# Kernel tuning notes

Hardware: AMD Instinct MI355X
Metric: run time of the kernel (lower is better)

## Reference

```python
import jax, jax.numpy as jnp
import numpy as np

# Lloyd-Max (Max 1960) optimal 16-level quantizer for N(0,1), bits=4
_CODEBOOK_4 = np.array([-2.7326, -2.069, -1.6181, -1.2562, -0.9424, -0.6568,
                        -0.3881, -0.1284, 0.1284, 0.3881, 0.6568, 0.9424,
                        1.2562, 1.6181, 2.069, 2.7326], dtype=np.float32)
DIM = 256


def setup_inputs() -> dict:
    key = jax.random.key(0)
    kx, kq = jax.random.split(key)
    x = jax.random.normal(kx, (4, 4096, DIM), dtype=jnp.float32)
    # orthogonal rotation via QR of a Gaussian matrix (mirrors torch.linalg.qr)
    rotation, _ = jnp.linalg.qr(jax.random.normal(kq, (DIM, DIM), dtype=jnp.float32))
    codebook = jnp.asarray(_CODEBOOK_4)
    return {"x": x, "rotation": rotation, "codebook": codebook}


def reference(x, rotation, codebook):
    shape = x.shape
    d = shape[-1]
    sqrt_d = jnp.sqrt(jnp.asarray(d, dtype=x.dtype))
    x_flat = x.reshape(-1, d)                                   # (N, d)
    x_norm = jnp.maximum(
        jnp.linalg.norm(x_flat, axis=-1, keepdims=True), 1e-8)  # (N, 1)
    u = x_flat / x_norm                                         # unit vectors
    y_scaled = (u @ rotation.T) * sqrt_d                        # ~N(0,1) coords
    # nearest codebook entry per scalar coordinate: (N, d, K) -> argmin over K
    idx = jnp.argmin(jnp.abs(y_scaled[..., None] - codebook), axis=-1)
    y_hat = codebook[idx] / sqrt_d                              # (N, d)
    x_hat = (y_hat @ rotation) * x_norm                         # de-rotate, rescale
    return x_hat.reshape(shape)
```

## Files before the change

### kernel.cpp

```cpp
#include <hip/hip_runtime.h>

typedef _Float16 f16;
typedef _Float16 f16x4 __attribute__((ext_vector_type(4)));
typedef _Float16 f16x8 __attribute__((ext_vector_type(8)));
typedef float f32x16 __attribute__((ext_vector_type(16)));
typedef float f32x4 __attribute__((ext_vector_type(4)));

#define APITCH 264

__global__ void prep_kernel(const float* __restrict__ R, f16* __restrict__ ws) {
  f16* W1h = ws;
  f16* W1l = ws + 65536;
  f16* W2h = ws + 131072;
  const int f = blockIdx.x;
  const int g = f >> 4, ks16 = f & 15;
  const int t = threadIdx.x;
  const int l = t >> 3, j = t & 7;
  const int col = 32 * g + (l & 31);
  const int k = 16 * ks16 + 8 * (l >> 5) + j;
  float v1 = R[col * 256 + k] * 256.0f;
  f16 h = (f16)v1;
  f16 lo = (f16)(v1 - (float)h);
  W1h[f * 512 + t] = h;
  W1l[f * 512 + t] = lo;
  W2h[f * 512 + t] = (f16)R[k * 256 + col];
}

__global__ __launch_bounds__(512, 4) void tq_main(
    const float* __restrict__ X, const float* __restrict__ CB,
    const f16* __restrict__ ws, float* __restrict__ OUT) {
  __shared__ f16 A1h[32][APITCH];
  __shared__ f16 A1l[32][APITCH];
  __shared__ float pn[16][32];
  __shared__ float s1s[32], s2s[32];

  const int tid = threadIdx.x;
  const int lane = tid & 63;
  const int wv = tid >> 6;
  const int lrow = lane & 31;
  const int kg = lane >> 5;
  const long row0 = (long)blockIdx.x * 32;

  const f16* W1h = ws;
  const f16* W1l = ws + 65536;
  const f16* W2h = ws + 131072;

  const int r = tid >> 4, q = tid & 15;
  const float* xp = X + (row0 + r) * 256 + q * 16;
  float xa[16];
  #pragma unroll
  for (int i = 0; i < 4; ++i) {
    f32x4 v = ((const f32x4*)xp)[i];
    xa[4 * i] = v.x; xa[4 * i + 1] = v.y; xa[4 * i + 2] = v.z; xa[4 * i + 3] = v.w;
  }
  float ss = 0.f;
  #pragma unroll
  for (int i = 0; i < 16; ++i) ss += xa[i] * xa[i];
  pn[q][r] = ss;
  __syncthreads();
  if (tid < 32) {
    float s = 0.f;
    #pragma unroll
    for (int i = 0; i < 16; ++i) s += pn[i][tid];
    float nrm = fmaxf(sqrtf(s), 1e-8f);
    s1s[tid] = 4096.0f / nrm;
    s2s[tid] = nrm * 0.0625f;
  }
  __syncthreads();

  {
    float s1f = s1s[r];
    #pragma unroll
    for (int c8 = 0; c8 < 2; ++c8) {
      f16x8 h, l;
      #pragma unroll
      for (int j = 0; j < 8; ++j) {
        float a = xa[c8 * 8 + j] * s1f;
        f16 hh = (f16)a;
        h[j] = hh;
        l[j] = (f16)(a - (float)hh);
      }
      *(f16x8*)&A1h[r][q * 16 + c8 * 8] = h;
      *(f16x8*)&A1l[r][q * 16 + c8 * 8] = l;
    }
  }
  __syncthreads();

  const int fb = wv * 16;
  const int lofs = lane * 8;
  f16x8 bh = *(const f16x8*)(W1h + fb * 512 + lofs);
  f16x8 bl = *(const f16x8*)(W1l + fb * 512 + lofs);
  f32x16 zv;
  #pragma unroll
  for (int i = 0; i < 16; ++i) zv[i] = 0.0f;
  f32x16 accH = zv, accL = zv;
  #pragma unroll 4
  for (int ks = 0; ks < 16; ++ks) {
    f16x8 cbh = bh, cbl = bl;
    if (ks < 15) {
      bh = *(const f16x8*)(W1h + (fb + ks + 1) * 512 + lofs);
      bl = *(const f16x8*)(W1l + (fb + ks + 1) * 512 + lofs);
    }
    const int k0 = ks * 16 + kg * 8;
    f16x8 ah = *(const f16x8*)&A1h[lrow][k0];
    f16x8 al = *(const f16x8*)&A1l[lrow][k0];
    accH = __builtin_amdgcn_mfma_f32_32x32x16_f16(ah, cbh, accH, 0, 0, 0);
    accL = __builtin_amdgcn_mfma_f32_32x32x16_f16(al, cbh, accL, 0, 0, 0);
    accH = __builtin_amdgcn_mfma_f32_32x32x16_f16(ah, cbl, accH, 0, 0, 0);
    accL = __builtin_amdgcn_mfma_f32_32x32x16_f16(al, cbl, accL, 0, 0, 0);
  }
  f32x16 acc;
  #pragma unroll
  for (int i = 0; i < 16; ++i) acc[i] = accH[i] + accL[i];

  __syncthreads();

  float cbf[16];
  #pragma unroll
  for (int i = 0; i < 16; ++i) cbf[i] = CB[i];
  float M[15];
  #pragma unroll
  for (int t = 0; t < 15; ++t) M[t] = 65536.0f * (0.5f * (cbf[t] + cbf[t + 1]));
  unsigned int cpk[8];
  #pragma unroll
  for (int i = 0; i < 8; ++i) {
    unsigned short lb = __builtin_bit_cast(unsigned short, (f16)cbf[2 * i]);
    unsigned short hb = __builtin_bit_cast(unsigned short, (f16)cbf[2 * i + 1]);
    cpk[i] = ((unsigned int)hb << 16) | (unsigned int)lb;
  }

  f16 (*Qs)[APITCH] = A1h;
  #pragma unroll
  for (int rr = 0; rr < 16; ++rr) {
    float y = acc[rr];
    int row = 4 * kg + (rr & 3) + 8 * (rr >> 2);
    int kk = 32 * wv + lrow;
    bool b3 = y > M[7];
    float m2 = b3 ? M[11] : M[3];
    bool b2 = y > m2;
    float m1 = b3 ? (b2 ? M[13] : M[9]) : (b2 ? M[5] : M[1]);
    bool b1 = y > m1;
    float m0 = b1 ? (b3 ? (b2 ? M[14] : M[10]) : (b2 ? M[6] : M[2]))
                  : (b3 ? (b2 ? M[12] : M[8]) : (b2 ? M[4] : M[0]));
    bool b0 = y > m0;
    unsigned int pp = b3 ? (b2 ? (b1 ? cpk[7] : cpk[6]) : (b1 ? cpk[5] : cpk[4]))
                         : (b2 ? (b1 ? cpk[3] : cpk[2]) : (b1 ? cpk[1] : cpk[0]));
    unsigned short qb = (unsigned short)(b0 ? (pp >> 16) : (pp & 0xFFFFu));
    Qs[row][kk] = __builtin_bit_cast(f16, qb);
  }
  __syncthreads();

  f16x8 b2 = *(const f16x8*)(W2h + fb * 512 + lofs);
  f32x16 acc2 = zv;
  #pragma unroll 4
  for (int ks = 0; ks < 16; ++ks) {
    f16x8 cb2 = b2;
    if (ks < 15) b2 = *(const f16x8*)(W2h + (fb + ks + 1) * 512 + lofs);
    f16x8 qa = *(const f16x8*)&Qs[lrow][ks * 16 + kg * 8];
    acc2 = __builtin_amdgcn_mfma_f32_32x32x16_f16(qa, cb2, acc2, 0, 0, 0);
  }

  #pragma unroll
  for (int rr = 0; rr < 16; ++rr) {
    int row = 4 * kg + (rr & 3) + 8 * (rr >> 2);
    int col = 32 * wv + lrow;
    OUT[(row0 + row) * 256 + col] = acc2[rr] * s2s[row];
  }
}

#define FB_APITCH 264
#define FB_B1PITCH 40
#define FB_B2PITCH 264

__global__ __launch_bounds__(256, 1) void tq_main_fb(
    const float* __restrict__ X, const float* __restrict__ R,
    const float* __restrict__ CB, float* __restrict__ OUT) {
  __shared__ f16 A1h[64][FB_APITCH];
  __shared__ f16 A1l[64][FB_APITCH];
  __shared__ f16 Qs[64][FB_APITCH];
  __shared__ f32x4 Braw[2624];
  __shared__ float pn[4][64];
  __shared__ float s1s[64];
  __shared__ float s2s[64];

  f16 (*B1h)[FB_B1PITCH] = (f16(*)[FB_B1PITCH])Braw;
  f16 (*B1l)[FB_B1PITCH] = (f16(*)[FB_B1PITCH])((char*)Braw + 20480);
  f16 (*B2h)[FB_B2PITCH] = (f16(*)[FB_B2PITCH])Braw;

  const int tid = threadIdx.x;
  const int lane = tid & 63;
  const int wv = tid >> 6;
  const int lrow = lane & 31;
  const int kg = lane >> 5;
  const long row0 = (long)blockIdx.x * 64;

  float cbf[16];
  #pragma unroll
  for (int i = 0; i < 16; ++i) cbf[i] = CB[i];
  float M[15];
  #pragma unroll
  for (int t = 0; t < 15; ++t) M[t] = 65536.0f * (0.5f * (cbf[t] + cbf[t + 1]));
  unsigned int cpk[8];
  #pragma unroll
  for (int i = 0; i < 8; ++i) {
    unsigned short lb = __builtin_bit_cast(unsigned short, (f16)cbf[2 * i]);
    unsigned short hb = __builtin_bit_cast(unsigned short, (f16)cbf[2 * i + 1]);
    cpk[i] = ((unsigned int)hb << 16) | (unsigned int)lb;
  }

  const int xrow = tid >> 2, xq = tid & 3;
  const float* xp = X + (row0 + xrow) * 256 + xq * 64;
  float xa[64];
  #pragma unroll
  for (int i = 0; i < 16; ++i) {
    f32x4 v = ((const f32x4*)xp)[i];
    xa[4 * i] = v.x; xa[4 * i + 1] = v.y; xa[4 * i + 2] = v.z; xa[4 * i + 3] = v.w;
  }
  float ss = 0.f;
  #pragma unroll
  for (int i = 0; i < 64; ++i) ss += xa[i] * xa[i];
  pn[xq][xrow] = ss;
  __syncthreads();
  if (tid < 64) {
    float s = pn[0][tid] + pn[1][tid] + pn[2][tid] + pn[3][tid];
    float nrm = fmaxf(sqrtf(s), 1e-8f);
    s1s[tid] = 4096.0f / nrm;
    s2s[tid] = nrm * 0.0625f;
  }
  __syncthreads();

  {
    float s1f = s1s[xrow];
    #pragma unroll
    for (int c8 = 0; c8 < 8; ++c8) {
      f16x8 h, l;
      #pragma unroll
      for (int j = 0; j < 8; ++j) {
        float a = xa[c8 * 8 + j] * s1f;
        f16 hh = (f16)a;
        h[j] = hh;
        l[j] = (f16)(a - (float)hh);
      }
      *(f16x8*)&A1h[xrow][xq * 64 + c8 * 8] = h;
      *(f16x8*)&A1l[xrow][xq * 64 + c8 * 8] = l;
    }
  }

  f32x4 pf[8];
  #pragma unroll
  for (int q = 0; q < 8; ++q) {
    int c = q * 256 + tid;
    pf[q] = *(const f32x4*)&R[(long)(c >> 3) * 256 + ((c & 7) * 4)];
  }

  f32x16 zv;
  #pragma unroll
  for (int i = 0; i < 16; ++i) zv[i] = 0.0f;
  f32x16 acc[2][2];
  acc[0][0] = zv; acc[0][1] = zv; acc[1][0] = zv; acc[1][1] = zv;

  for (int kp = 0; kp < 8; ++kp) {
    __syncthreads();
    #pragma unroll
    for (int q = 0; q < 8; ++q) {
      int c = q * 256 + tid;
      int n = c >> 3, k4 = (c & 7) * 4;
      f16x4 h, l;
      #pragma unroll
      for (int j = 0; j < 4; ++j) {
        float sv = pf[q][j] * 256.0f;
        f16 hh = (f16)sv;
        h[j] = hh;
        l[j] = (f16)(sv - (float)hh);
      }
      *(f16x4*)&B1h[n][k4] = h;
      *(f16x4*)&B1l[n][k4] = l;
    }
    __syncthreads();
    if (kp < 7) {
      #pragma unroll
      for (int q = 0; q < 8; ++q) {
        int c = q * 256 + tid;
        pf[q] = *(const f32x4*)&R[(long)(c >> 3) * 256 + (kp + 1) * 32 + ((c & 7) * 4)];
      }
    }
    #pragma unroll
    for (int ks = 0; ks < 2; ++ks) {
      const int k0 = kp * 32 + ks * 16 + kg * 8;
      const int lk = ks * 16 + kg * 8;
      f16x8 ah[2], al[2], bhf[2], blf[2];
      #pragma unroll
      for (int m = 0; m < 2; ++m) {
        ah[m] = *(const f16x8*)&A1h[32 * m + lrow][k0];
        al[m] = *(const f16x8*)&A1l[32 * m + lrow][k0];
      }
      #pragma unroll
      for (int n = 0; n < 2; ++n) {
        int col = 64 * wv + 32 * n + lrow;
        bhf[n] = *(const f16x8*)&B1h[col][lk];
        blf[n] = *(const f16x8*)&B1l[col][lk];
      }
      #pragma unroll
      for (int m = 0; m < 2; ++m)
        #pragma unroll
        for (int n = 0; n < 2; ++n) {
          acc[m][n] = __builtin_amdgcn_mfma_f32_32x32x16_f16(ah[m], bhf[n], acc[m][n], 0, 0, 0);
          acc[m][n] = __builtin_amdgcn_mfma_f32_32x32x16_f16(al[m], bhf[n], acc[m][n], 0, 0, 0);
          acc[m][n] = __builtin_amdgcn_mfma_f32_32x32x16_f16(ah[m], blf[n], acc[m][n], 0, 0, 0);
          acc[m][n] = __builtin_amdgcn_mfma_f32_32x32x16_f16(al[m], blf[n], acc[m][n], 0, 0, 0);
        }
    }
  }

  #pragma unroll
  for (int q = 0; q < 8; ++q) {
    int c = q * 256 + tid;
    pf[q] = *(const f32x4*)&R[(long)(c >> 6) * 256 + ((c & 63) * 4)];
  }

  #pragma unroll
  for (int m = 0; m < 2; ++m)
    #pragma unroll
    for (int n = 0; n < 2; ++n)
      #pragma unroll
      for (int rr = 0; rr < 16; ++rr) {
        float y = acc[m][n][rr];
        int row = 32 * m + 4 * kg + (rr & 3) + 8 * (rr >> 2);
        int kk = 64 * wv + 32 * n + lrow;
        bool b3 = y > M[7];
        float m2 = b3 ? M[11] : M[3];
        bool b2 = y > m2;
        float m1 = b3 ? (b2 ? M[13] : M[9]) : (b2 ? M[5] : M[1]);
        bool b1 = y > m1;
        float m0 = b1 ? (b3 ? (b2 ? M[14] : M[10]) : (b2 ? M[6] : M[2]))
                      : (b3 ? (b2 ? M[12] : M[8]) : (b2 ? M[4] : M[0]));
        bool b0 = y > m0;
        unsigned int pp = b3 ? (b2 ? (b1 ? cpk[7] : cpk[6]) : (b1 ? cpk[5] : cpk[4]))
                             : (b2 ? (b1 ? cpk[3] : cpk[2]) : (b1 ? cpk[1] : cpk[0]));
        unsigned short qb = (unsigned short)(b0 ? (pp >> 16) : (pp & 0xFFFFu));
        Qs[row][kk] = __builtin_bit_cast(f16, qb);
      }
  __syncthreads();

  f32x16 acc2[2][2];
  acc2[0][0] = zv; acc2[0][1] = zv; acc2[1][0] = zv; acc2[1][1] = zv;

  for (int kp = 0; kp < 8; ++kp) {
    if (kp) __syncthreads();
    #pragma unroll
    for (int q = 0; q < 8; ++q) {
      int c = q * 256 + tid;
      int k = c >> 6, n4 = (c & 63) * 4;
      f16x4 h;
      #pragma unroll
      for (int j = 0; j < 4; ++j) h[j] = (f16)pf[q][j];
      *(f16x4*)&B2h[k][n4] = h;
    }
    __syncthreads();
    if (kp < 7) {
      #pragma unroll
      for (int q = 0; q < 8; ++q) {
        int c = q * 256 + tid;
        pf[q] = *(const f32x4*)&R[(long)((kp + 1) * 32 + (c >> 6)) * 256 + ((c & 63) * 4)];
      }
    }
    #pragma unroll
    for (int ks = 0; ks < 2; ++ks) {
      const int k0 = kp * 32 + ks * 16 + kg * 8;
      const int lk = ks * 16 + kg * 8;
      f16x8 qa[2], bb[2];
      #pragma unroll
      for (int m = 0; m < 2; ++m) qa[m] = *(const f16x8*)&Qs[32 * m + lrow][k0];
      #pragma unroll
      for (int n = 0; n < 2; ++n) {
        int colg = 64 * wv + 32 * n + lrow;
        #pragma unroll
        for (int j = 0; j < 8; ++j) bb[n][j] = B2h[lk + j][colg];
      }
      #pragma unroll
      for (int m = 0; m < 2; ++m)
        #pragma unroll
        for (int n = 0; n < 2; ++n)
          acc2[m][n] = __builtin_amdgcn_mfma_f32_32x32x16_f16(qa[m], bb[n], acc2[m][n], 0, 0, 0);
    }
  }

  #pragma unroll
  for (int m = 0; m < 2; ++m)
    #pragma unroll
    for (int n = 0; n < 2; ++n)
      #pragma unroll
      for (int rr = 0; rr < 16; ++rr) {
        int row = 32 * m + 4 * kg + (rr & 3) + 8 * (rr >> 2);
        int col = 64 * wv + 32 * n + lrow;
        OUT[(row0 + row) * 256 + col] = acc2[m][n][rr] * s2s[row];
      }
}

extern "C" void kernel_launch(void* const* d_in, const int* in_sizes, int n_in,
                              void* d_out, int out_size, void* d_ws, size_t ws_size,
                              hipStream_t stream) {
  const float* X = (const float*)d_in[0];
  const float* R = (const float*)d_in[1];
  const float* CB = (const float*)d_in[2];
  float* OUT = (float*)d_out;
  const int nrows = in_sizes[0] / 256;

  if (ws_size >= 3u * 65536u * sizeof(f16)) {
    f16* ws = (f16*)d_ws;
    prep_kernel<<<128, 512, 0, stream>>>(R, ws);
    tq_main<<<nrows / 32, 512, 0, stream>>>(X, CB, ws, OUT);
  } else {
    tq_main_fb<<<nrows / 64, 256, 0, stream>>>(X, R, CB, OUT);
  }
}
```

Before: 28.13 us.

## Restage prep via LDS, shuffle row norms, deepen weight prefetch with dual accumulators

The prep kernel now stages 32 rotation rows in shared memory and writes the fragmented f16 weights with vector stores. It runs 8 blocks of 1024 threads, and the workspace regions are padded so the prefetch can run past the end. The main kernel computes row norms with wave shuffles instead of a shared-memory reduction, which removes two barriers. It also fully unrolls both MFMA loops with two- and four-deep weight prefetch, issues the second GEMM's weight loads before the quantize phase, and splits the second GEMM across two accumulators to break the dependency chain. The cost is more registers and extra reads into the padding past each weight region.

```diff
diff --git a/kernel.cpp b/kernel.cpp
--- a/kernel.cpp
+++ b/kernel.cpp
@@ -7,23 +7,53 @@
 typedef float f32x4 __attribute__((ext_vector_type(4)));
 
 #define APITCH 264
-
-__global__ void prep_kernel(const float* __restrict__ R, f16* __restrict__ ws) {
+#define WREG 67584
+
+__global__ __launch_bounds__(1024) void prep_kernel(const float* __restrict__ R,
+                                                    f16* __restrict__ ws) {
+  __shared__ float Lrs[32][260];
+  const int g = blockIdx.x;
+  const int t = threadIdx.x;
   f16* W1h = ws;
-  f16* W1l = ws + 65536;
-  f16* W2h = ws + 131072;
-  const int f = blockIdx.x;
-  const int g = f >> 4, ks16 = f & 15;
-  const int t = threadIdx.x;
-  const int l = t >> 3, j = t & 7;
-  const int col = 32 * g + (l & 31);
-  const int k = 16 * ks16 + 8 * (l >> 5) + j;
-  float v1 = R[col * 256 + k] * 256.0f;
-  f16 h = (f16)v1;
-  f16 lo = (f16)(v1 - (float)h);
-  W1h[f * 512 + t] = h;
-  W1l[f * 512 + t] = lo;
-  W2h[f * 512 + t] = (f16)R[k * 256 + col];
+  f16* W1l = ws + WREG;
+  f16* W2h = ws + 2 * WREG;
+
+  #pragma unroll
+  for (int it = 0; it < 2; ++it) {
+    int c = it * 1024 + t;
+    int row = c >> 6, c4 = (c & 63) * 4;
+    f32x4 v = *(const f32x4*)&R[(long)(32 * g + row) * 256 + c4];
+    *(f32x4*)&Lrs[row][c4] = v;
+  }
+  __syncthreads();
+
+  {
+    int f_loc = t >> 6, l = t & 63;
+    int k0 = 16 * f_loc + 8 * (l >> 5);
+    const float* src = &Lrs[l & 31][k0];
+    f16x8 h, lo;
+    #pragma unroll
+    for (int j = 0; j < 8; ++j) {
+      float v = src[j] * 256.0f;
+      f16 hh = (f16)v;
+      h[j] = hh;
+      lo[j] = (f16)(v - (float)hh);
+    }
+    long o = (long)(g * 16 + f_loc) * 512 + l * 8;
+    *(f16x8*)(W1h + o) = h;
+    *(f16x8*)(W1l + o) = lo;
+  }
+
+  {
+    int gp = t >> 7, e = (t >> 6) & 1, l = t & 63;
+    int lr0 = 16 * e + 8 * (l >> 5);
+    int col = 32 * gp + (l & 31);
+    f16x8 h;
+    #pragma unroll
+    for (int j = 0; j < 8; ++j) h[j] = (f16)Lrs[lr0 + j][col];
+    long o = (long)(gp * 16 + 2 * g + e) * 512 + l * 8;
+    *(f16x8*)(W2h + o) = h;
+  }
 }
 
 __global__ __launch_bounds__(512, 4) void tq_main(
@@ -31,8 +61,7 @@
     const f16* __restrict__ ws, float* __restrict__ OUT) {
   __shared__ f16 A1h[32][APITCH];
   __shared__ f16 A1l[32][APITCH];
-  __shared__ float pn[16][32];
-  __shared__ float s1s[32], s2s[32];
+  __shared__ float s2s[32];
 
   const int tid = threadIdx.x;
   const int lane = tid & 63;
@@ -42,8 +71,8 @@
   const long row0 = (long)blockIdx.x * 32;
 
   const f16* W1h = ws;
-  const f16* W1l = ws + 65536;
-  const f16* W2h = ws + 131072;
+  const f16* W1l = ws + WREG;
+  const f16* W2h = ws + 2 * WREG;
 
   const int r = tid >> 4, q = tid & 15;
   const float* xp = X + (row0 + r) * 256 + q * 16;
@@ -56,62 +85,75 @@
   float ss = 0.f;
   #pragma unroll
   for (int i = 0; i < 16; ++i) ss += xa[i] * xa[i];
-  pn[q][r] = ss;
-  __syncthreads();
-  if (tid < 32) {
-    float s = 0.f;
-    #pragma unroll
-    for (int i = 0; i < 16; ++i) s += pn[i][tid];
-    float nrm = fmaxf(sqrtf(s), 1e-8f);
-    s1s[tid] = 4096.0f / nrm;
-    s2s[tid] = nrm * 0.0625f;
-  }
-  __syncthreads();
-
-  {
-    float s1f = s1s[r];
-    #pragma unroll
-    for (int c8 = 0; c8 < 2; ++c8) {
-      f16x8 h, l;
-      #pragma unroll
-      for (int j = 0; j < 8; ++j) {
-        float a = xa[c8 * 8 + j] * s1f;
-        f16 hh = (f16)a;
-        h[j] = hh;
-        l[j] = (f16)(a - (float)hh);
-      }
-      *(f16x8*)&A1h[r][q * 16 + c8 * 8] = h;
-      *(f16x8*)&A1l[r][q * 16 + c8 * 8] = l;
-    }
-  }
-  __syncthreads();
-
-  const int fb = wv * 16;
-  const int lofs = lane * 8;
-  f16x8 bh = *(const f16x8*)(W1h + fb * 512 + lofs);
-  f16x8 bl = *(const f16x8*)(W1l + fb * 512 + lofs);
+  ss += __shfl_xor(ss, 8, 16);
+  ss += __shfl_xor(ss, 4, 16);
+  ss += __shfl_xor(ss, 2, 16);
+  ss += __shfl_xor(ss, 1, 16);
+  float nrm = fmaxf(sqrtf(ss), 1e-8f);
+  float s1f = 4096.0f / nrm;
+  if (q == 0) s2s[r] = nrm * 0.0625f;
+
+  #pragma unroll
+  for (int c8 = 0; c8 < 2; ++c8) {
+    f16x8 h, l;
+    #pragma unroll
+    for (int j = 0; j < 8; ++j) {
+      float a = xa[c8 * 8 + j] * s1f;
+      f16 hh = (f16)a;
+      h[j] = hh;
+      l[j] = (f16)(a - (float)hh);
+    }
+    *(f16x8*)&A1h[r][q * 16 + c8 * 8] = h;
+    *(f16x8*)&A1l[r][q * 16 + c8 * 8] = l;
+  }
+  __syncthreads();
+
+  const f16* W1hp = W1h + (long)(wv * 16) * 512 + lane * 8;
+  const f16* W1lp = W1l + (long)(wv * 16) * 512 + lane * 8;
+  f16x8 bh0 = *(const f16x8*)(W1hp);
+  f16x8 bl0 = *(const f16x8*)(W1lp);
+  f16x8 bh1 = *(const f16x8*)(W1hp + 512);
+  f16x8 bl1 = *(const f16x8*)(W1lp + 512);
+
   f32x16 zv;
   #pragma unroll
   for (int i = 0; i < 16; ++i) zv[i] = 0.0f;
   f32x16 accH = zv, accL = zv;
-  #pragma unroll 4
-  for (int ks = 0; ks < 16; ++ks) {
-    f16x8 cbh = bh, cbl = bl;
-    if (ks < 15) {
-      bh = *(const f16x8*)(W1h + (fb + ks + 1) * 512 + lofs);
-      bl = *(const f16x8*)(W1l + (fb + ks + 1) * 512 + lofs);
-    }
-    const int k0 = ks * 16 + kg * 8;
-    f16x8 ah = *(const f16x8*)&A1h[lrow][k0];
-    f16x8 al = *(const f16x8*)&A1l[lrow][k0];
-    accH = __builtin_amdgcn_mfma_f32_32x32x16_f16(ah, cbh, accH, 0, 0, 0);
-    accL = __builtin_amdgcn_mfma_f32_32x32x16_f16(al, cbh, accL, 0, 0, 0);
-    accH = __builtin_amdgcn_mfma_f32_32x32x16_f16(ah, cbl, accH, 0, 0, 0);
-    accL = __builtin_amdgcn_mfma_f32_32x32x16_f16(al, cbl, accL, 0, 0, 0);
+
+  #pragma unroll
+  for (int ks = 0; ks < 16; ks += 2) {
+    {
+      const int k0 = ks * 16 + kg * 8;
+      f16x8 ah = *(const f16x8*)&A1h[lrow][k0];
+      f16x8 al = *(const f16x8*)&A1l[lrow][k0];
+      accH = __builtin_amdgcn_mfma_f32_32x32x16_f16(ah, bh0, accH, 0, 0, 0);
+      accL = __builtin_amdgcn_mfma_f32_32x32x16_f16(al, bh0, accL, 0, 0, 0);
+      accH = __builtin_amdgcn_mfma_f32_32x32x16_f16(ah, bl0, accH, 0, 0, 0);
+      accL = __builtin_amdgcn_mfma_f32_32x32x16_f16(al, bl0, accL, 0, 0, 0);
+      bh0 = *(const f16x8*)(W1hp + (ks + 2) * 512);
+      bl0 = *(const f16x8*)(W1lp + (ks + 2) * 512);
+    }
+    {
+      const int k0 = (ks + 1) * 16 + kg * 8;
+      f16x8 ah = *(const f16x8*)&A1h[lrow][k0];
+      f16x8 al = *(const f16x8*)&A1l[lrow][k0];
+      accH = __builtin_amdgcn_mfma_f32_32x32x16_f16(ah, bh1, accH, 0, 0, 0);
+      accL = __builtin_amdgcn_mfma_f32_32x32x16_f16(al, bh1, accL, 0, 0, 0);
+      accH = __builtin_amdgcn_mfma_f32_32x32x16_f16(ah, bl1, accH, 0, 0, 0);
+      accL = __builtin_amdgcn_mfma_f32_32x32x16_f16(al, bl1, accL, 0, 0, 0);
+      bh1 = *(const f16x8*)(W1hp + (ks + 3) * 512);
+      bl1 = *(const f16x8*)(W1lp + (ks + 3) * 512);
+    }
   }
   f32x16 acc;
   #pragma unroll
   for (int i = 0; i < 16; ++i) acc[i] = accH[i] + accL[i];
+
+  const f16* W2p = W2h + (long)(wv * 16) * 512 + lane * 8;
+  f16x8 c0 = *(const f16x8*)(W2p);
+  f16x8 c1 = *(const f16x8*)(W2p + 512);
+  f16x8 c2 = *(const f16x8*)(W2p + 1024);
+  f16x8 c3 = *(const f16x8*)(W2p + 1536);
 
   __syncthreads();
 
@@ -150,21 +192,36 @@
   }
   __syncthreads();
 
-  f16x8 b2 = *(const f16x8*)(W2h + fb * 512 + lofs);
-  f32x16 acc2 = zv;
-  #pragma unroll 4
-  for (int ks = 0; ks < 16; ++ks) {
-    f16x8 cb2 = b2;
-    if (ks < 15) b2 = *(const f16x8*)(W2h + (fb + ks + 1) * 512 + lofs);
-    f16x8 qa = *(const f16x8*)&Qs[lrow][ks * 16 + kg * 8];
-    acc2 = __builtin_amdgcn_mfma_f32_32x32x16_f16(qa, cb2, acc2, 0, 0, 0);
+  f32x16 acc2a = zv, acc2b = zv;
+  #pragma unroll
+  for (int ks = 0; ks < 16; ks += 4) {
+    {
+      f16x8 qa = *(const f16x8*)&Qs[lrow][ks * 16 + kg * 8];
+      acc2a = __builtin_amdgcn_mfma_f32_32x32x16_f16(qa, c0, acc2a, 0, 0, 0);
+      c0 = *(const f16x8*)(W2p + (ks + 4) * 512);
+    }
+    {
+      f16x8 qa = *(const f16x8*)&Qs[lrow][(ks + 1) * 16 + kg * 8];
+      acc2b = __builtin_amdgcn_mfma_f32_32x32x16_f16(qa, c1, acc2b, 0, 0, 0);
+      c1 = *(const f16x8*)(W2p + (ks + 5) * 512);
+    }
+    {
+      f16x8 qa = *(const f16x8*)&Qs[lrow][(ks + 2) * 16 + kg * 8];
+      acc2a = __builtin_amdgcn_mfma_f32_32x32x16_f16(qa, c2, acc2a, 0, 0, 0);
+      c2 = *(const f16x8*)(W2p + (ks + 6) * 512);
+    }
+    {
+      f16x8 qa = *(const f16x8*)&Qs[lrow][(ks + 3) * 16 + kg * 8];
+      acc2b = __builtin_amdgcn_mfma_f32_32x32x16_f16(qa, c3, acc2b, 0, 0, 0);
+      c3 = *(const f16x8*)(W2p + (ks + 7) * 512);
+    }
   }
 
   #pragma unroll
   for (int rr = 0; rr < 16; ++rr) {
     int row = 4 * kg + (rr & 3) + 8 * (rr >> 2);
     int col = 32 * wv + lrow;
-    OUT[(row0 + row) * 256 + col] = acc2[rr] * s2s[row];
+    OUT[(row0 + row) * 256 + col] = (acc2a[rr] + acc2b[rr]) * s2s[row];
   }
 }
 
@@ -406,9 +463,9 @@
   float* OUT = (float*)d_out;
   const int nrows = in_sizes[0] / 256;
 
-  if (ws_size >= 3u * 65536u * sizeof(f16)) {
+  if (ws_size >= (size_t)3 * WREG * sizeof(f16)) {
     f16* ws = (f16*)d_ws;
-    prep_kernel<<<128, 512, 0, stream>>>(R, ws);
+    prep_kernel<<<8, 1024, 0, stream>>>(R, ws);
     tq_main<<<nrows / 32, 512, 0, stream>>>(X, CB, ws, OUT);
   } else {
     tq_main_fb<<<nrows / 64, 256, 0, stream>>>(X, R, CB, OUT);
```

Result: faster. 27.13 us (-3.5%).
